# Optimization experiments

Measured on AMD Instinct MI355X. Metric: run time of the kernel, lower is better.

Reference implementation:

```python
import jax, jax.numpy as jnp
import numpy as np

HEADS = 2
K_HOP = 2
RATIO = 0.8
NEG_SLOPE = 0.01


def seg_softmax(logits, seg, num_seg):
    # torch_geometric.utils.softmax: numerically stable segment softmax
    m = jax.ops.segment_max(logits, seg, num_segments=num_seg)
    e = jnp.exp(logits - m[seg])
    d = jax.ops.segment_sum(e, seg, num_segments=num_seg)
    return e / d[seg]


def _attention(key_value, query, seg, num_seg, Wk, W1, W2, W3):
    # Attention.forward with enable_BN=False; weights stored [in,out] so x@W == torch Linear
    a = key_value @ Wk
    h = jnp.concatenate([a, query, a - query, a * query], axis=-1)  # [N,4H]
    h = jax.nn.leaky_relu(h @ W1, NEG_SLOPE)
    h = jax.nn.leaky_relu(h @ W2, NEG_SLOPE)
    h = jax.nn.leaky_relu(h @ W3, NEG_SLOPE)  # [N,1]
    return seg_softmax(h[:, 0], seg, num_seg)[:, None]  # att_weights [N,1]


def setup_inputs():
    key = jax.random.key(0)
    ks = jax.random.split(key, 10)
    B, n, H, epg = 64, 64, 128, 2048
    N = B * n
    x = jax.random.normal(ks[0], (N, H), jnp.float32)
    src = jax.random.randint(ks[1], (B, epg), 0, n)
    dst = jax.random.randint(ks[2], (B, epg), 0, n)
    off = (jnp.arange(B) * n)[:, None]
    edge_index = jnp.stack([(src + off).reshape(-1), (dst + off).reshape(-1)], 0)
    edge_weight = jax.random.uniform(ks[3], (B * epg,), jnp.float32)
    target_x = jax.random.normal(ks[4], (B, H), jnp.float32)
    batch_ixs = jnp.repeat(jnp.arange(B), n)
    s = lambda i, sh: jax.random.normal(ks[i], sh, jnp.float32) / np.sqrt(sh[-2])
    # index 0=cluster_att, 1=query_att, 2=cluster_att2, 3=query_att2
    att_Wk = s(5, (4, H, H))
    att_W1 = s(6, (4, 4 * H, 2 * H))
    att_W2 = s(7, (4, 2 * H, H))
    att_W3 = s(8, (4, H, 1))
    lin_W = s(9, (HEADS, H, H))
    return dict(x=x, edge_index=edge_index, edge_weight=edge_weight, target_x=target_x,
                batch_ixs=batch_ixs, att_Wk=att_Wk, att_W1=att_W1, att_W2=att_W2,
                att_W3=att_W3, lin_W=lin_W)


def reference(x, edge_index, edge_weight, target_x, batch_ixs, att_Wk, att_W1, att_W2, att_W3, lin_W):
    N, H = x.shape
    B = target_x.shape[0]
    n = N // B
    # ---- gcn_norm with self loops (fill 1.0) ----
    loop = jnp.arange(N)
    row = jnp.concatenate([edge_index[0], loop])
    col = jnp.concatenate([edge_index[1], loop])
    w = jnp.concatenate([edge_weight, jnp.ones((N,), edge_weight.dtype)])
    deg = jax.ops.segment_sum(w, col, num_segments=N)
    dinv = jnp.where(deg > 0, jax.lax.rsqrt(jnp.maximum(deg, 1e-12)), 0.0)
    ew = dinv[row] * w * dinv[col]  # [L]
    # ---- k-hop propagation ----
    def hop(v):
        return jax.ops.segment_sum(v[row] * ew[:, None], col, num_segments=N)
    x_q = x
    for _ in range(K_HOP):
        x_q = hop(x_q)
    qt = target_x[batch_ixs]  # repeat_interleave by per-graph counts (sorted batch)
    # ---- multi-head edge attention (reuse_att_w=True, dropout=0 -> E identical per head) ----
    f1 = _attention(x, x_q, batch_ixs, B, att_Wk[0], att_W1[0], att_W2[0], att_W3[0])
    f2 = _attention(x, qt, batch_ixs, B, att_Wk[1], att_W1[1], att_W2[1], att_W3[1])
    E = jax.nn.leaky_relu(f1[col] + f2[row], NEG_SLOPE)  # [L,1]
    E = seg_softmax(E[:, 0], col, N)[:, None]
    x_c = jnp.zeros_like(x)
    E_g = jnp.zeros((row.shape[0], 1), x.dtype)
    agg = jax.ops.segment_sum(x[row] * E, col, num_segments=N)
    for h in range(HEADS):
        x_c = x_c + jax.nn.leaky_relu(x + agg @ lin_W[h], NEG_SLOPE)
        E_g = E_g + E
    x_c = x_c / HEADS
    E_g = E_g / HEADS
    # ---- second k-hop + cluster scoring ----
    x_q2 = x_c
    for _ in range(K_HOP):
        x_q2 = hop(x_q2)
    g1 = _attention(x_c, x_q2, batch_ixs, B, att_Wk[2], att_W1[2], att_W2[2], att_W3[2])
    g2 = _attention(x_c, qt, batch_ixs, B, att_Wk[3], att_W1[3], att_W2[3], att_W3[3])
    # stack over heads then mean == g1+g2 (same attention modules reused per head)
    cluster_score = seg_softmax((g1 + g2)[:, 0], batch_ixs, B)  # [N]
    # ---- per-graph topk (ratio) ----
    kk = int(np.ceil(RATIO * n))
    _, idx = jax.lax.top_k(cluster_score.reshape(B, n), kk)  # descending, matches PyG topk
    perm = (idx + (jnp.arange(B) * n)[:, None]).reshape(-1)  # [Nk]
    x_out = x[perm] * cluster_score[perm][:, None]
    batch_out = batch_ixs[perm]
    # ---- S^T A S (dense equivalent of SparseTensor triple product) ----
    A_d = jnp.zeros((N, N), x.dtype).at[row, col].add(ew)
    S_d = jnp.zeros((N, N), x.dtype).at[row, col].add(E_g[:, 0])
    S_p = S_d[:, perm]  # S[:, perm] -> [N, Nk]
    A2 = S_p.T @ (A_d @ S_p)  # [Nk, Nk]
    Nk = perm.shape[0]
    A2 = A2.at[jnp.arange(Nk), jnp.arange(Nk)].set(1.0)  # fill_diag(1.0)
    return x_out, A2, batch_out, perm
```

## Files before the change

kernel.cpp:

```cpp
#include <hip/hip_runtime.h>

#define KK 52
#define NKOUT 3328
#define NEG 0.01f

typedef __attribute__((ext_vector_type(8))) __bf16 bf16x8;
typedef __attribute__((ext_vector_type(16))) float floatx16;

__device__ __forceinline__ float lrelu(float v){ return v > 0.f ? v : NEG*v; }

#define SW(r, ko) ((r)*40 + ((ko) ^ ((((r)>>3)&3) << 3)))

__device__ __forceinline__ void split_store8(const float* vv, __bf16* P0, __bf16* P1, __bf16* P2, int addr){
  bf16x8 p1, p2, p3;
  #pragma unroll
  for (int j = 0; j < 8; j++){
    __bf16 b1 = (__bf16)vv[j];
    float r1 = vv[j] - (float)b1;
    __bf16 b2 = (__bf16)r1;
    float r2 = r1 - (float)b2;
    p1[j] = b1; p2[j] = b2; p3[j] = (__bf16)r2;
  }
  *(bf16x8*)(P0 + addr) = p1;
  *(bf16x8*)(P1 + addr) = p2;
  *(bf16x8*)(P2 + addr) = p3;
}

__device__ __forceinline__ void mfma6(const __bf16* A0, const __bf16* A1, const __bf16* A2,
                                      const __bf16* B0, const __bf16* B1, const __bf16* B2,
                                      int aoff, int boff, floatx16* acc){
  bf16x8 a1 = *(const bf16x8*)(A0 + aoff);
  bf16x8 a2 = *(const bf16x8*)(A1 + aoff);
  bf16x8 a3 = *(const bf16x8*)(A2 + aoff);
  bf16x8 b1 = *(const bf16x8*)(B0 + boff);
  bf16x8 b2 = *(const bf16x8*)(B1 + boff);
  bf16x8 b3 = *(const bf16x8*)(B2 + boff);
  floatx16 c = *acc;
  c = __builtin_amdgcn_mfma_f32_32x32x16_bf16(a1,b1,c,0,0,0);
  c = __builtin_amdgcn_mfma_f32_32x32x16_bf16(a1,b2,c,0,0,0);
  c = __builtin_amdgcn_mfma_f32_32x32x16_bf16(a2,b1,c,0,0,0);
  c = __builtin_amdgcn_mfma_f32_32x32x16_bf16(a1,b3,c,0,0,0);
  c = __builtin_amdgcn_mfma_f32_32x32x16_bf16(a3,b1,c,0,0,0);
  c = __builtin_amdgcn_mfma_f32_32x32x16_bf16(a2,b2,c,0,0,0);
  *acc = c;
}

__device__ __forceinline__ void g_gemm(const float* A0, int ldA,
                                       const float* __restrict__ W0, int ldW, int K,
                                       __bf16* pb, floatx16* oA, floatx16* oB){
  __bf16 *As0 = pb, *As1 = pb+2560, *As2 = pb+5120;
  __bf16 *Bs0 = pb+7680, *Bs1 = pb+12800, *Bs2 = pb+17920;
  int tid = threadIdx.x;
  int sar = tid >> 2, sako = (tid & 3)*8;
  int bn = tid & 127, bk = (tid >> 7)*16;
  int wv_ = tid >> 6, L = tid & 63, m = L & 31, half = L >> 5;
  int rA = 32*(wv_ & 1) + m, rB0 = (wv_ >> 1)*32 + m, rB1 = rB0 + 64;
  const float* arow = A0 + (size_t)sar*ldA;
  floatx16 accA, accB;
  #pragma unroll
  for (int i = 0; i < 16; i++){ accA[i] = 0.f; accB[i] = 0.f; }
  float ra[8], wv[16];
  {
    float4 v0 = *(const float4*)(arow + sako);
    float4 v1 = *(const float4*)(arow + sako + 4);
    ra[0]=v0.x; ra[1]=v0.y; ra[2]=v0.z; ra[3]=v0.w; ra[4]=v1.x; ra[5]=v1.y; ra[6]=v1.z; ra[7]=v1.w;
    #pragma unroll
    for (int j = 0; j < 16; j++) wv[j] = W0[(size_t)(bk + j)*ldW + bn];
  }
  for (int k0 = 0; k0 < K; k0 += 32){
    split_store8(ra, As0, As1, As2, SW(sar, sako));
    split_store8(wv,     Bs0, Bs1, Bs2, SW(bn, bk));
    split_store8(wv + 8, Bs0, Bs1, Bs2, SW(bn, bk + 8));
    __syncthreads();
    int k1 = k0 + 32;
    float ra2[8], wv2[16];
    if (k1 < K){
      float4 v0 = *(const float4*)(arow + k1 + sako);
      float4 v1 = *(const float4*)(arow + k1 + sako + 4);
      ra2[0]=v0.x; ra2[1]=v0.y; ra2[2]=v0.z; ra2[3]=v0.w; ra2[4]=v1.x; ra2[5]=v1.y; ra2[6]=v1.z; ra2[7]=v1.w;
      #pragma unroll
      for (int j = 0; j < 16; j++) wv2[j] = W0[(size_t)(k1 + bk + j)*ldW + bn];
    }
    #pragma unroll
    for (int kg = 0; kg < 2; kg++){
      int ko = kg*16 + half*8;
      mfma6(As0,As1,As2, Bs0,Bs1,Bs2, SW(rA,ko), SW(rB0,ko), &accA);
      mfma6(As0,As1,As2, Bs0,Bs1,Bs2, SW(rA,ko), SW(rB1,ko), &accB);
    }
    __syncthreads();
    if (k1 < K){
      #pragma unroll
      for (int j = 0; j < 8; j++) ra[j] = ra2[j];
      #pragma unroll
      for (int j = 0; j < 16; j++) wv[j] = wv2[j];
    }
  }
  *oA = accA; *oB = accB;
}

__device__ __forceinline__ void g_gemm64_bp(const float* __restrict__ A0, int ldA,
                                            const __bf16* __restrict__ Bp, int bps, int ldKb, int K,
                                            __bf16* pb, floatx16* oC){
  __bf16 *As0 = pb, *As1 = pb+2560, *As2 = pb+5120;
  __bf16 *Bs0 = pb+7680, *Bs1 = pb+10240, *Bs2 = pb+12800;
  int tid = threadIdx.x;
  int sar = tid >> 2, sako = (tid & 3)*8;
  int bn = tid & 63, bk = (tid >> 6)*8;
  int wv_ = tid >> 6, L = tid & 63, m = L & 31, half = L >> 5;
  int rA = 32*(wv_ & 1) + m, rB = 32*(wv_ >> 1) + m;
  const float* arow = A0 + (size_t)sar*ldA;
  const __bf16* brow = Bp + (size_t)bn*ldKb + bk;
  floatx16 acc;
  #pragma unroll
  for (int i = 0; i < 16; i++) acc[i] = 0.f;
  float ra[8]; bf16x8 rb[3];
  {
    float4 v0 = *(const float4*)(arow + sako);
    float4 v1 = *(const float4*)(arow + sako + 4);
    ra[0]=v0.x; ra[1]=v0.y; ra[2]=v0.z; ra[3]=v0.w; ra[4]=v1.x; ra[5]=v1.y; ra[6]=v1.z; ra[7]=v1.w;
    rb[0] = *(const bf16x8*)(brow);
    rb[1] = *(const bf16x8*)(brow + bps);
    rb[2] = *(const bf16x8*)(brow + 2*bps);
  }
  for (int k0 = 0; k0 < K; k0 += 32){
    split_store8(ra, As0, As1, As2, SW(sar, sako));
    *(bf16x8*)(Bs0 + SW(bn, bk)) = rb[0];
    *(bf16x8*)(Bs1 + SW(bn, bk)) = rb[1];
    *(bf16x8*)(Bs2 + SW(bn, bk)) = rb[2];
    __syncthreads();
    int k1 = k0 + 32;
    float ra2[8]; bf16x8 rb2[3];
    if (k1 < K){
      float4 v0 = *(const float4*)(arow + k1 + sako);
      float4 v1 = *(const float4*)(arow + k1 + sako + 4);
      ra2[0]=v0.x; ra2[1]=v0.y; ra2[2]=v0.z; ra2[3]=v0.w; ra2[4]=v1.x; ra2[5]=v1.y; ra2[6]=v1.z; ra2[7]=v1.w;
      rb2[0] = *(const bf16x8*)(brow + k1);
      rb2[1] = *(const bf16x8*)(brow + bps + k1);
      rb2[2] = *(const bf16x8*)(brow + 2*bps + k1);
    }
    #pragma unroll
    for (int kg = 0; kg < 2; kg++){
      int ko = kg*16 + half*8;
      mfma6(As0,As1,As2, Bs0,Bs1,Bs2, SW(rA,ko), SW(rB,ko), &acc);
    }
    __syncthreads();
    if (k1 < K){
      #pragma unroll
      for (int j = 0; j < 8; j++) ra[j] = ra2[j];
      rb[0]=rb2[0]; rb[1]=rb2[1]; rb[2]=rb2[2];
    }
  }
  *oC = acc;
}

__device__ __forceinline__ void g_gemm_h64(const float* __restrict__ arow, const float* __restrict__ qrow,
                                           const __bf16* __restrict__ Bp,
                                           __bf16* pb, floatx16* oC){
  __bf16 *As0 = pb, *As1 = pb+2560, *As2 = pb+5120;
  __bf16 *Bs0 = pb+7680, *Bs1 = pb+10240, *Bs2 = pb+12800;
  int tid = threadIdx.x;
  int sar = tid >> 2, sako = (tid & 3)*8;
  int bn = tid & 63, bk = (tid >> 6)*8;
  int wv_ = tid >> 6, L = tid & 63, m = L & 31, half = L >> 5;
  int rA = 32*(wv_ & 1) + m, rB = 32*(wv_ >> 1) + m;
  const __bf16* brow = Bp + (size_t)bn*384 + bk;
  auto loadA = [&](int k0, float* r){
    int seg = k0 >> 7, kl = (k0 & 127) + sako;
    if (seg == 0){
      float4 a0 = *(const float4*)(arow + kl), a1 = *(const float4*)(arow + kl + 4);
      r[0]=a0.x; r[1]=a0.y; r[2]=a0.z; r[3]=a0.w; r[4]=a1.x; r[5]=a1.y; r[6]=a1.z; r[7]=a1.w;
    } else if (seg == 1){
      float4 q0 = *(const float4*)(qrow + kl), q1 = *(const float4*)(qrow + kl + 4);
      r[0]=q0.x; r[1]=q0.y; r[2]=q0.z; r[3]=q0.w; r[4]=q1.x; r[5]=q1.y; r[6]=q1.z; r[7]=q1.w;
    } else {
      float4 a0 = *(const float4*)(arow + kl), a1 = *(const float4*)(arow + kl + 4);
      float4 q0 = *(const float4*)(qrow + kl), q1 = *(const float4*)(qrow + kl + 4);
      r[0]=a0.x*q0.x; r[1]=a0.y*q0.y; r[2]=a0.z*q0.z; r[3]=a0.w*q0.w;
      r[4]=a1.x*q1.x; r[5]=a1.y*q1.y; r[6]=a1.z*q1.z; r[7]=a1.w*q1.w;
    }
  };
  floatx16 acc;
  #pragma unroll
  for (int i = 0; i < 16; i++) acc[i] = 0.f;
  float ra[8]; bf16x8 rb[3];
  loadA(0, ra);
  rb[0] = *(const bf16x8*)(brow);
  rb[1] = *(const bf16x8*)(brow + 98304);
  rb[2] = *(const bf16x8*)(brow + 196608);
  for (int k0 = 0; k0 < 384; k0 += 32){
    split_store8(ra, As0, As1, As2, SW(sar, sako));
    *(bf16x8*)(Bs0 + SW(bn, bk)) = rb[0];
    *(bf16x8*)(Bs1 + SW(bn, bk)) = rb[1];
    *(bf16x8*)(Bs2 + SW(bn, bk)) = rb[2];
    __syncthreads();
    int k1 = k0 + 32;
    float ra2[8]; bf16x8 rb2[3];
    if (k1 < 384){
      loadA(k1, ra2);
      rb2[0] = *(const bf16x8*)(brow + k1);
      rb2[1] = *(const bf16x8*)(brow + 98304 + k1);
      rb2[2] = *(const bf16x8*)(brow + 196608 + k1);
    }
    #pragma unroll
    for (int kg = 0; kg < 2; kg++){
      int ko = kg*16 + half*8;
      mfma6(As0,As1,As2, Bs0,Bs1,Bs2, SW(rA,ko), SW(rB,ko), &acc);
    }
    __syncthreads();
    if (k1 < 384){
      #pragma unroll
      for (int j = 0; j < 8; j++) ra[j] = ra2[j];
      rb[0]=rb2[0]; rb[1]=rb2[1]; rb[2]=rb2[2];
    }
  }
  *oC = acc;
}

__device__ __forceinline__ void c_write(floatx16 accA, floatx16 accB, float* C0, int ldC, int act){
  int tid = threadIdx.x, wv_ = tid >> 6, L = tid & 63, m = L & 31, half = L >> 5;
  int rB0 = (wv_ >> 1)*32 + m, rB1 = rB0 + 64;
  int row0 = 32*(wv_ & 1) + 4*half;
  #pragma unroll
  for (int reg = 0; reg < 16; reg++){
    int row = row0 + (reg & 3) + 8*(reg >> 2);
    float va = accA[reg], vb = accB[reg];
    if (act){ va = lrelu(va); vb = lrelu(vb); }
    C0[(size_t)row*ldC + rB0] = va;
    C0[(size_t)row*ldC + rB1] = vb;
  }
}

__device__ __forceinline__ void c_write64(floatx16 acc, float* C0, int ldC, int act){
  int tid = threadIdx.x, wv_ = tid >> 6, L = tid & 63, m = L & 31, half = L >> 5;
  int col = 32*(wv_ >> 1) + m;
  int row0 = 32*(wv_ & 1) + 4*half;
  #pragma unroll
  for (int reg = 0; reg < 16; reg++){
    int row = row0 + (reg & 3) + 8*(reg >> 2);
    float v = acc[reg];
    if (act) v = lrelu(v);
    C0[(size_t)row*ldC + col] = v;
  }
}

__device__ __forceinline__ void hop2_run(const float* A, const float* VfullL, int ldV,
                                         const float* srcG, float* dstG, int dstOff,
                                         float* Vt, float* Tt, int fbeg, int fend){
  int tid = threadIdx.x;
  int tc = (tid & 31)*2, tf = (tid >> 5)*4;
  for (int f0 = fbeg; f0 < fend; f0 += 32){
    if (!VfullL){
      for (int o = tid; o < 2048; o += 256){
        int r = o >> 5, f = o & 31;
        Vt[o] = srcG[r*128 + f0 + f];
      }
      __syncthreads();
    }
    float a00,a01,a02,a03,a10,a11,a12,a13;
    a00=a01=a02=a03=a10=a11=a12=a13=0.f;
    for (int r = 0; r < 64; r++){
      float x0 = A[r*64 + tc], x1 = A[r*64 + tc + 1];
      float4 v4 = VfullL ? *(const float4*)&VfullL[r*ldV + f0 + tf]
                         : *(const float4*)&Vt[r*32 + tf];
      a00 += x0*v4.x; a01 += x0*v4.y; a02 += x0*v4.z; a03 += x0*v4.w;
      a10 += x1*v4.x; a11 += x1*v4.y; a12 += x1*v4.z; a13 += x1*v4.w;
    }
    *(float4*)&Tt[tc*32 + tf]     = make_float4(a00,a01,a02,a03);
    *(float4*)&Tt[(tc+1)*32 + tf] = make_float4(a10,a11,a12,a13);
    __syncthreads();
    a00=a01=a02=a03=a10=a11=a12=a13=0.f;
    for (int r = 0; r < 64; r++){
      float x0 = A[r*64 + tc], x1 = A[r*64 + tc + 1];
      float4 v4 = *(const float4*)&Tt[r*32 + tf];
      a00 += x0*v4.x; a01 += x0*v4.y; a02 += x0*v4.z; a03 += x0*v4.w;
      a10 += x1*v4.x; a11 += x1*v4.y; a12 += x1*v4.z; a13 += x1*v4.w;
    }
    *(float4*)(dstG + tc*128 + dstOff + f0 + tf)     = make_float4(a00,a01,a02,a03);
    *(float4*)(dstG + (tc+1)*128 + dstOff + f0 + tf) = make_float4(a10,a11,a12,a13);
    __syncthreads();
  }
}

__device__ __forceinline__ void split_t_lds(float v, __bf16* Ls, int idx){
  __bf16 b1 = (__bf16)v;
  float r1 = v - (float)b1;
  __bf16 b2 = (__bf16)r1;
  __bf16 b3 = (__bf16)(r1 - (float)b2);
  Ls[idx] = b1; Ls[4224 + idx] = b2; Ls[8448 + idx] = b3;
}

__global__ __launch_bounds__(256) void k_p0(const int* __restrict__ ei, const float* __restrict__ ew,
                                            const float* __restrict__ x, const float* __restrict__ Wk,
                                            const float* __restrict__ W1, const float* __restrict__ W2,
                                            const float* __restrict__ linW,
                                            float* A_g, float* M_g, float* xq, float* a_buf,
                                            __bf16* W1fp, __bf16* W2p, __bf16* Wkgp,
                                            float* xl0, float* xl1, float* outA2){
  __shared__ __align__(16) char POOL[57856];
  float* pf = (float*)POOL;
  __bf16* pb = (__bf16*)POOL;
  int blk = blockIdx.x, tid = threadIdx.x;
  if (blk < 128){
    int b = blk >> 1, fh = blk & 1;
    float* Ws = pf; float* Mc = pf + 4096; float* dv = pf + 8192;
    for (int i = tid; i < 4096; i += 256){ Ws[i] = 0.f; Mc[i] = 0.f; }
    __syncthreads();
    const int* r0 = ei + b*2048;
    const int* c0 = ei + 64*2048 + b*2048;
    const float* w0 = ew + b*2048;
    int base = b*64;
    for (int e = tid; e < 2048; e += 256){
      int r = r0[e] - base, c = c0[e] - base;
      atomicAdd(&Ws[r*64 + c], w0[e]);
      atomicAdd(&Mc[r*64 + c], 1.f);
    }
    if (tid < 64){ atomicAdd(&Ws[tid*65], 1.f); atomicAdd(&Mc[tid*65], 1.f); }
    __syncthreads();
    if (tid < 64){
      float d = 0.f;
      for (int r = 0; r < 64; r++) d += Ws[r*64 + tid];
      dv[tid] = d > 0.f ? rsqrtf(fmaxf(d, 1e-12f)) : 0.f;
    }
    __syncthreads();
    for (int i = tid; i < 4096; i += 256){
      int r = i >> 6, c = i & 63;
      float a = dv[r]*Ws[i]*dv[c];
      Ws[i] = a;
      if (fh == 0){
        A_g[b*4096 + i] = a;
        M_g[b*4096 + i] = Mc[i];
      }
    }
    __syncthreads();
    hop2_run(Ws, nullptr, 0, x + (size_t)b*8192, xq + (size_t)b*8192, 0, pf + 8256, pf + 10304,
             fh*64, fh*64 + 64);
  } else if (blk < 256){
    int idx = blk - 128, z = idx >> 6, b = idx & 63;
    floatx16 cA, cB;
    g_gemm(x + (size_t)b*8192, 128, Wk + (size_t)z*16384, 128, 128, pb, &cA, &cB);
    c_write(cA, cB, a_buf + (size_t)z*524288 + (size_t)b*8192, 128, 0);
  } else if (blk < 352){
    __bf16* Ls = (__bf16*)POOL;
    int t = blk - 256, z = t/24, tt = t%24, k0 = (tt >> 2)*64, c0 = (tt & 3)*64;
    const float* Wz = W1 + (size_t)z*131072;
    for (int i = tid; i < 4096; i += 256){
      int kk = i >> 6, cc = i & 63, kr = k0 + kk, c = c0 + cc;
      float v;
      if (kr < 128)       v = Wz[kr*256 + c] + Wz[(kr + 256)*256 + c];
      else if (kr < 256)  v = Wz[kr*256 + c] - Wz[(kr + 128)*256 + c];
      else                v = Wz[(kr + 128)*256 + c];
      split_t_lds(v, Ls, cc*66 + kk);
    }
    __syncthreads();
    __bf16* outp = W1fp + (size_t)z*294912;
    for (int i = tid; i < 4096; i += 256){
      int cc = i >> 6, kk = i & 63;
      int o = (c0 + cc)*384 + k0 + kk;
      int li = cc*66 + kk;
      outp[o] = Ls[li];
      outp[98304 + o] = Ls[4224 + li];
      outp[196608 + o] = Ls[8448 + li];
    }
  } else if (blk < 384){
    __bf16* Ls = (__bf16*)POOL;
    int t = blk - 352, z = t >> 3, tt = t & 7, k0 = (tt >> 1)*64, c0 = (tt & 1)*64;
    const float* Wz = W2 + (size_t)z*32768;
    for (int i = tid; i < 4096; i += 256){
      int kk = i >> 6, cc = i & 63;
      split_t_lds(Wz[(k0 + kk)*128 + c0 + cc], Ls, cc*66 + kk);
    }
    __syncthreads();
    __bf16* outp = W2p + (size_t)z*98304;
    for (int i = tid; i < 4096; i += 256){
      int cc = i >> 6, kk = i & 63;
      int o = (c0 + cc)*256 + k0 + kk;
      int li = cc*66 + kk;
      outp[o] = Ls[li];
      outp[32768 + o] = Ls[4224 + li];
      outp[65536 + o] = Ls[8448 + li];
    }
  } else if (blk < 392){
    __bf16* Ls = (__bf16*)POOL;
    int t = blk - 384, z = t >> 2, tt = t & 3, k0 = (tt >> 1)*64, c0 = (tt & 1)*64;
    const float* Wz = Wk + (size_t)(2 + z)*16384;
    for (int i = tid; i < 4096; i += 256){
      int kk = i >> 6, cc = i & 63;
      split_t_lds(Wz[(k0 + kk)*128 + c0 + cc], Ls, cc*66 + kk);
    }
    __syncthreads();
    __bf16* outp = Wkgp + (size_t)z*49152;
    for (int i = tid; i < 4096; i += 256){
      int cc = i >> 6, kk = i & 63;
      int o = (c0 + cc)*128 + k0 + kk;
      int li = cc*66 + kk;
      outp[o] = Ls[li];
      outp[16384 + o] = Ls[4224 + li];
      outp[32768 + o] = Ls[8448 + li];
    }
  } else if (blk < 3096){
    float4* p = (float4*)outA2;
    int base = (blk - 392)*1024 + tid;
    #pragma unroll
    for (int i = 0; i < 4; i++) p[base + i*256] = make_float4(0.f,0.f,0.f,0.f);
  } else {
    int idx = blk - 3096, z = idx >> 6, b = idx & 63;
    floatx16 cA, cB;
    g_gemm(x + (size_t)b*8192, 128, linW + (size_t)z*16384, 128, 128, pb, &cA, &cB);
    c_write(cA, cB, (z ? xl1 : xl0) + (size_t)b*8192, 128, 0);
  }
}

__global__ __launch_bounds__(256) void k_h1(const float* __restrict__ a_buf, const float* __restrict__ q0,
                                            const float* __restrict__ tgt, const __bf16* __restrict__ W1fp,
                                            float* h1){
  __shared__ __align__(16) char POOL[30720];
  __bf16* pb = (__bf16*)POOL;
  int blk = blockIdx.x, tid = threadIdx.x;
  int b = blk >> 3, z = (blk >> 2) & 1, nq = blk & 3;
  int sar = tid >> 2;
  const float* arow = a_buf + (size_t)z*524288 + ((size_t)b*64 + sar)*128;
  const float* qrow = z ? (tgt + (size_t)b*128) : (q0 + ((size_t)b*64 + sar)*128);
  floatx16 c;
  g_gemm_h64(arow, qrow, W1fp + (size_t)z*294912 + (size_t)nq*64*384, pb, &c);
  c_write64(c, h1 + (size_t)z*1048576 + (size_t)b*16384 + nq*64, 256, 1);
}

__global__ __launch_bounds__(256) void k_w2p(const float* __restrict__ h1, const __bf16* __restrict__ W2p,
                                             const float* __restrict__ W3, float* __restrict__ lp){
  __shared__ __align__(16) char POOL[30720];
  __shared__ float lgp[128];
  __bf16* pb = (__bf16*)POOL;
  int blk = blockIdx.x, tid = threadIdx.x;
  int b = blk >> 2, z = (blk >> 1) & 1, nh = blk & 1;
  floatx16 c;
  g_gemm64_bp(h1 + (size_t)z*1048576 + (size_t)b*16384, 256,
              W2p + (size_t)z*98304 + (size_t)nh*64*256, 32768, 256, 256, pb, &c);
  int wv_ = tid >> 6, L = tid & 63, m = L & 31, half = L >> 5;
  int col = 32*(wv_ >> 1) + m;
  float w = W3[z*128 + nh*64 + col];
  float v[16];
  #pragma unroll
  for (int reg = 0; reg < 16; reg++) v[reg] = lrelu(c[reg])*w;
  #pragma unroll
  for (int off = 1; off < 32; off <<= 1)
    #pragma unroll
    for (int reg = 0; reg < 16; reg++) v[reg] += __shfl_xor(v[reg], off);
  if (m == 0){
    #pragma unroll
    for (int reg = 0; reg < 16; reg++) lgp[wv_*32 + half*16 + reg] = v[reg];
  }
  __syncthreads();
  if (tid < 64){
    int row = tid, rh = row >> 5, rem = row & 31;
    int hf = (rem >> 2) & 1, rg = (rem & 3) + 4*(rem >> 3);
    float p = lgp[rh*32 + hf*16 + rg] + lgp[(rh + 2)*32 + hf*16 + rg];
    lp[(z*2 + nh)*4096 + b*64 + row] = p;
  }
}

__global__ __launch_bounds__(256) void k_edgehop(const float* __restrict__ M_g, const float* __restrict__ lp,
                                                 const float* __restrict__ x, const float* __restrict__ xl0g,
                                                 const float* __restrict__ xl1g, const float* __restrict__ A_g,
                                                 float* S_g, float* xcb, float* xq2){
  __shared__ __align__(16) float Mc[4096];
  __shared__ __align__(16) float xh[4096];
  __shared__ __align__(16) float xl0h[4096];
  __shared__ __align__(16) float xl1h[4096];
  __shared__ __align__(16) float Ab[4096];
  __shared__ __align__(16) float Tt[2048];
  __shared__ float f1s[64], f2s[64];
  int blk = blockIdx.x, b = blk >> 1, fh = blk & 1, tid = threadIdx.x;
  int foff = fh*64;
  for (int i = tid; i < 4096; i += 256) Mc[i] = M_g[b*4096 + i];
  for (int o = tid*4; o < 4096; o += 1024){
    int r = o >> 6, f = o & 63;
    *(float4*)&xh[o]   = *(const float4*)(x    + (size_t)b*8192 + r*128 + foff + f);
    *(float4*)&xl0h[o] = *(const float4*)(xl0g + (size_t)b*8192 + r*128 + foff + f);
    *(float4*)&xl1h[o] = *(const float4*)(xl1g + (size_t)b*8192 + r*128 + foff + f);
  }
  if (tid < 128){
    int z = tid >> 6, r = tid & 63;
    float d = lp[(z*2)*4096 + b*64 + r] + lp[(z*2 + 1)*4096 + b*64 + r];
    float l = lrelu(d);
    float mx = l;
    #pragma unroll
    for (int off = 32; off; off >>= 1) mx = fmaxf(mx, __shfl_xor(mx, off));
    float e = expf(l - mx);
    float s = e;
    #pragma unroll
    for (int off = 32; off; off >>= 1) s += __shfl_xor(s, off);
    (z ? f2s : f1s)[r] = e/s;
  }
  __syncthreads();
  {
    int c = tid >> 2, sub = tid & 3;
    float m = -1e30f;
    for (int r = sub; r < 64; r += 4)
      if (Mc[r*64 + c] > 0.f) m = fmaxf(m, lrelu(f1s[c] + f2s[r]));
    m = fmaxf(m, __shfl_xor(m, 1));
    m = fmaxf(m, __shfl_xor(m, 2));
    float s = 0.f;
    for (int r = sub; r < 64; r += 4){
      float mc = Mc[r*64 + c];
      if (mc > 0.f) s += mc*expf(lrelu(f1s[c] + f2s[r]) - m);
    }
    s += __shfl_xor(s, 1);
    s += __shfl_xor(s, 2);
    for (int r = sub; r < 64; r += 4){
      float mc = Mc[r*64 + c];
      float v = 0.f;
      if (mc > 0.f) v = mc*expf(lrelu(f1s[c] + f2s[r]) - m)/s;
      Mc[r*64 + c] = v;
    }
  }
  __syncthreads();
  if (fh == 0)
    for (int i = tid; i < 4096; i += 256) S_g[b*4096 + i] = Mc[i];
  {
    int tc = (tid & 15)*4, tf = (tid >> 4)*4;
    float a0[4][4], a1[4][4];
    #pragma unroll
    for (int i = 0; i < 4; i++)
      #pragma unroll
      for (int j = 0; j < 4; j++){ a0[i][j] = 0.f; a1[i][j] = 0.f; }
    for (int r = 0; r < 64; r++){
      float4 e4 = *(const float4*)&Mc[r*64 + tc];
      float4 p0 = *(const float4*)&xl0h[r*64 + tf];
      float4 p1 = *(const float4*)&xl1h[r*64 + tf];
      float e_[4] = {e4.x,e4.y,e4.z,e4.w};
      float p0_[4] = {p0.x,p0.y,p0.z,p0.w};
      float p1_[4] = {p1.x,p1.y,p1.z,p1.w};
      #pragma unroll
      for (int ci = 0; ci < 4; ci++)
        #pragma unroll
        for (int fj = 0; fj < 4; fj++){
          a0[ci][fj] += e_[ci]*p0_[fj];
          a1[ci][fj] += e_[ci]*p1_[fj];
        }
    }
    __syncthreads();
    #pragma unroll
    for (int ci = 0; ci < 4; ci++){
      int c = tc + ci;
      float4 xv = *(const float4*)&xh[c*64 + tf];
      float4 o;
      o.x = 0.5f*(lrelu(xv.x + a0[ci][0]) + lrelu(xv.x + a1[ci][0]));
      o.y = 0.5f*(lrelu(xv.y + a0[ci][1]) + lrelu(xv.y + a1[ci][1]));
      o.z = 0.5f*(lrelu(xv.z + a0[ci][2]) + lrelu(xv.z + a1[ci][2]));
      o.w = 0.5f*(lrelu(xv.w + a0[ci][3]) + lrelu(xv.w + a1[ci][3]));
      *(float4*)&xh[c*64 + tf] = o;
      *(float4*)(xcb + (size_t)b*8192 + c*128 + foff + tf) = o;
    }
  }
  for (int i = tid*4; i < 4096; i += 1024)
    *(float4*)&Ab[i] = *(const float4*)(A_g + b*4096 + i);
  __syncthreads();
  hop2_run(Ab, xh, 64, nullptr, xq2 + (size_t)b*8192, foff, Tt, Tt, 0, 64);
}

__global__ __launch_bounds__(256) void k_wkg(const float* __restrict__ xcb, const __bf16* __restrict__ Wkgp,
                                             float* a_buf){
  __shared__ __align__(16) char POOL[30720];
  __bf16* pb = (__bf16*)POOL;
  int blk = blockIdx.x;
  int b = blk >> 2, z = (blk >> 1) & 1, nh = blk & 1;
  floatx16 c;
  g_gemm64_bp(xcb + (size_t)b*8192, 128,
              Wkgp + (size_t)z*49152 + (size_t)nh*64*128, 16384, 128, 128, pb, &c);
  c_write64(c, a_buf + (size_t)z*524288 + (size_t)b*8192 + nh*64, 128, 0);
}

__global__ __launch_bounds__(256) void k_A2c(const float* __restrict__ lp, const float* __restrict__ x,
                                             const float* __restrict__ A_g, const float* __restrict__ S_g,
                                             float* outA2, float* outX, float* outB, float* outP){
  __shared__ __align__(16) float At[64*68];
  __shared__ __align__(16) float Sp[64*56];
  __shared__ __align__(16) float Tq[64*56];
  __shared__ int pi[64];
  __shared__ float pv[64];
  int b = blockIdx.x, tid = threadIdx.x;
  if (tid < 64){
    int lane = tid;
    float f[2];
    #pragma unroll
    for (int z = 0; z < 2; z++){
      float d = lp[(z*2)*4096 + b*64 + lane] + lp[(z*2 + 1)*4096 + b*64 + lane];
      float l = lrelu(d);
      float mx = l;
      #pragma unroll
      for (int off = 32; off; off >>= 1) mx = fmaxf(mx, __shfl_xor(mx, off));
      float e = expf(l - mx);
      float sm = e;
      #pragma unroll
      for (int off = 32; off; off >>= 1) sm += __shfl_xor(sm, off);
      f[z] = e/sm;
    }
    float l = f[0] + f[1];
    float m = l;
    #pragma unroll
    for (int off = 32; off; off >>= 1) m = fmaxf(m, __shfl_xor(m, off));
    float e = expf(l - m);
    float sm = e;
    #pragma unroll
    for (int off = 32; off; off >>= 1) sm += __shfl_xor(sm, off);
    float v = e/sm;
    int idx = lane;
    #pragma unroll
    for (int k = 2; k <= 64; k <<= 1){
      #pragma unroll
      for (int j = k >> 1; j > 0; j >>= 1){
        float ov = __shfl_xor(v, j);
        int   oi = __shfl_xor(idx, j);
        bool ascBlock = (lane & k) == 0;
        bool iAmLow   = (lane & j) == 0;
        bool otherPrec = (ov > v) || (ov == v && oi < idx);
        bool take = (ascBlock == iAmLow) ? otherPrec : !otherPrec;
        if (take){ v = ov; idx = oi; }
      }
    }
    pi[lane] = idx; pv[lane] = v;
    if (lane < KK){
      outB[b*KK + lane] = (float)b;
      outP[b*KK + lane] = (float)(b*64 + idx);
    }
  }
  __syncthreads();
  for (int o = tid*4; o < KK*128; o += 1024){
    int j = o >> 7, f = o & 127;
    float4 xv = *(const float4*)(x + ((size_t)b*64 + pi[j])*128 + f);
    float sv = pv[j];
    *(float4*)(outX + (size_t)b*KK*128 + o) = make_float4(xv.x*sv, xv.y*sv, xv.z*sv, xv.w*sv);
  }
  for (int idx = tid; idx < 4096; idx += 256){
    int i = idx >> 6, k = idx & 63;
    At[k*68 + i] = A_g[b*4096 + idx];
  }
  for (int idx = tid; idx < 4096; idx += 256){
    int k = idx >> 6, t = idx & 63;
    if (t < 56) Sp[k*56 + t] = (t < KK) ? S_g[b*4096 + k*64 + pi[t]] : 0.f;
  }
  __syncthreads();
  if (tid < 224){
    int i0 = (tid/14)*4, t0 = (tid % 14)*4;
    float acc[4][4];
    #pragma unroll
    for (int a = 0; a < 4; a++)
      #pragma unroll
      for (int c = 0; c < 4; c++) acc[a][c] = 0.f;
    for (int k = 0; k < 64; k++){
      float4 a4 = *(const float4*)&At[k*68 + i0];
      float4 s4 = *(const float4*)&Sp[k*56 + t0];
      float a_[4] = {a4.x,a4.y,a4.z,a4.w};
      float s_[4] = {s4.x,s4.y,s4.z,s4.w};
      #pragma unroll
      for (int ii = 0; ii < 4; ii++)
        #pragma unroll
        for (int tt = 0; tt < 4; tt++) acc[ii][tt] += a_[ii]*s_[tt];
    }
    #pragma unroll
    for (int ii = 0; ii < 4; ii++)
      *(float4*)&Tq[(i0+ii)*56 + t0] = make_float4(acc[ii][0],acc[ii][1],acc[ii][2],acc[ii][3]);
  }
  __syncthreads();
  if (tid < 169){
    int a0 = (tid/13)*4, t0 = (tid % 13)*4;
    float acc[4][4];
    #pragma unroll
    for (int a = 0; a < 4; a++)
      #pragma unroll
      for (int c = 0; c < 4; c++) acc[a][c] = 0.f;
    for (int i = 0; i < 64; i++){
      float4 s4 = *(const float4*)&Sp[i*56 + a0];
      float4 t4 = *(const float4*)&Tq[i*56 + t0];
      float s_[4] = {s4.x,s4.y,s4.z,s4.w};
      float t_[4] = {t4.x,t4.y,t4.z,t4.w};
      #pragma unroll
      for (int aa = 0; aa < 4; aa++)
        #pragma unroll
        for (int tt = 0; tt < 4; tt++) acc[aa][tt] += s_[aa]*t_[tt];
    }
    #pragma unroll
    for (int aa = 0; aa < 4; aa++){
      int a = a0 + aa;
      float4 o;
      o.x = (a == t0    ) ? 1.f : acc[aa][0];
      o.y = (a == t0 + 1) ? 1.f : acc[aa][1];
      o.z = (a == t0 + 2) ? 1.f : acc[aa][2];
      o.w = (a == t0 + 3) ? 1.f : acc[aa][3];
      *(float4*)(outA2 + (size_t)(b*KK + a)*NKOUT + b*KK + t0) = o;
    }
  }
}

extern "C" void kernel_launch(void* const* d_in, const int* in_sizes, int n_in,
                              void* d_out, int out_size, void* d_ws, size_t ws_size,
                              hipStream_t stream){
  const float* x    = (const float*)d_in[0];
  const int*   ei   = (const int*)d_in[1];
  const float* ew   = (const float*)d_in[2];
  const float* tgt  = (const float*)d_in[3];
  const float* Wk   = (const float*)d_in[5];
  const float* W1   = (const float*)d_in[6];
  const float* W2   = (const float*)d_in[7];
  const float* W3   = (const float*)d_in[8];
  const float* linW = (const float*)d_in[9];
  float* out = (float*)d_out;

  float* wf   = (float*)d_ws;
  float* A_g  = wf;
  float* M_g  = wf + 262144;
  float* S_g  = wf + 524288;
  float* xq   = wf + 786432;
  float* xq2  = wf + 1310720;
  float* xl0  = wf + 1835008;
  float* xcb  = wf + 2359296;
  float* a_buf= wf + 2883584;
  float* h1   = wf + 3932160;
  float* lp   = wf + 6029312;
  float* xl1  = wf + 6045696;
  __bf16* W1fp = (__bf16*)(wf + 6569984);
  __bf16* W2p  = (__bf16*)(wf + 7159808);
  __bf16* Wkgp = (__bf16*)(wf + 7356416);

  float* outX  = out;
  float* outA2 = out + 425984;
  float* outB  = out + 425984 + 11075584;
  float* outP  = outB + NKOUT;

  k_p0<<<dim3(3224), dim3(256), 0, stream>>>(ei, ew, x, Wk, W1, W2, linW, A_g, M_g, xq, a_buf,
                                             W1fp, W2p, Wkgp, xl0, xl1, outA2);
  k_h1<<<dim3(512), dim3(256), 0, stream>>>(a_buf, xq, tgt, W1fp, h1);
  k_w2p<<<dim3(256), dim3(256), 0, stream>>>(h1, W2p, W3, lp);
  k_edgehop<<<dim3(128), dim3(256), 0, stream>>>(M_g, lp, x, xl0, xl1, A_g, S_g, xcb, xq2);
  k_wkg<<<dim3(256), dim3(256), 0, stream>>>(xcb, Wkgp, a_buf);
  k_h1<<<dim3(512), dim3(256), 0, stream>>>(a_buf, xq2, tgt, W1fp + 2*294912, h1);
  k_w2p<<<dim3(256), dim3(256), 0, stream>>>(h1, W2p + 2*98304, W3 + 2*128, lp);
  k_A2c<<<dim3(64), dim3(256), 0, stream>>>(lp, x, A_g, S_g, outA2, outX, outB, outP);
}
```

Measured before the change: 214.7 us.

## Fuse Wk projection of cluster features into edgehop kernel, drop k_wkg launch

The separate k_wkg GEMM launch is removed. Each edgehop block now multiplies its 64-feature half of the cluster features by the packed Wk weights with register-resident split-bf16 MFMA and writes a partial product. The second k_h1 sums the two feature-half partials while loading its A operand, so xcb no longer round-trips through memory and one launch is saved. The cost is extra partial-buffer traffic, an extra load in k_h1, and extra MFMA work and register pressure inside the low-occupancy edgehop kernel (128 blocks).

```diff
diff --git a/kernel.cpp b/kernel.cpp
--- a/kernel.cpp
+++ b/kernel.cpp
@@ -26,6 +26,19 @@
   *(bf16x8*)(P2 + addr) = p3;
 }
 
+__device__ __forceinline__ void split8r(const float* vv, bf16x8* q1, bf16x8* q2, bf16x8* q3){
+  bf16x8 p1, p2, p3;
+  #pragma unroll
+  for (int j = 0; j < 8; j++){
+    __bf16 b1 = (__bf16)vv[j];
+    float r1 = vv[j] - (float)b1;
+    __bf16 b2 = (__bf16)r1;
+    float r2 = r1 - (float)b2;
+    p1[j] = b1; p2[j] = b2; p3[j] = (__bf16)r2;
+  }
+  *q1 = p1; *q2 = p2; *q3 = p3;
+}
+
 __device__ __forceinline__ void mfma6(const __bf16* A0, const __bf16* A1, const __bf16* A2,
                                       const __bf16* B0, const __bf16* B1, const __bf16* B2,
                                       int aoff, int boff, floatx16* acc){
@@ -35,6 +48,18 @@
   bf16x8 b1 = *(const bf16x8*)(B0 + boff);
   bf16x8 b2 = *(const bf16x8*)(B1 + boff);
   bf16x8 b3 = *(const bf16x8*)(B2 + boff);
+  floatx16 c = *acc;
+  c = __builtin_amdgcn_mfma_f32_32x32x16_bf16(a1,b1,c,0,0,0);
+  c = __builtin_amdgcn_mfma_f32_32x32x16_bf16(a1,b2,c,0,0,0);
+  c = __builtin_amdgcn_mfma_f32_32x32x16_bf16(a2,b1,c,0,0,0);
+  c = __builtin_amdgcn_mfma_f32_32x32x16_bf16(a1,b3,c,0,0,0);
+  c = __builtin_amdgcn_mfma_f32_32x32x16_bf16(a3,b1,c,0,0,0);
+  c = __builtin_amdgcn_mfma_f32_32x32x16_bf16(a2,b2,c,0,0,0);
+  *acc = c;
+}
+
+__device__ __forceinline__ void mfma6r(bf16x8 a1, bf16x8 a2, bf16x8 a3,
+                                       bf16x8 b1, bf16x8 b2, bf16x8 b3, floatx16* acc){
   floatx16 c = *acc;
   c = __builtin_amdgcn_mfma_f32_32x32x16_bf16(a1,b1,c,0,0,0);
   c = __builtin_amdgcn_mfma_f32_32x32x16_bf16(a1,b2,c,0,0,0);
@@ -153,7 +178,8 @@
   *oC = acc;
 }
 
-__device__ __forceinline__ void g_gemm_h64(const float* __restrict__ arow, const float* __restrict__ qrow,
+__device__ __forceinline__ void g_gemm_h64(const float* arow, const float* arow2,
+                                           const float* __restrict__ qrow,
                                            const __bf16* __restrict__ Bp,
                                            __bf16* pb, floatx16* oC){
   __bf16 *As0 = pb, *As1 = pb+2560, *As2 = pb+5120;
@@ -164,19 +190,28 @@
   int wv_ = tid >> 6, L = tid & 63, m = L & 31, half = L >> 5;
   int rA = 32*(wv_ & 1) + m, rB = 32*(wv_ >> 1) + m;
   const __bf16* brow = Bp + (size_t)bn*384 + bk;
+  auto loadAv = [&](int kl, float* r){
+    float4 a0 = *(const float4*)(arow + kl), a1 = *(const float4*)(arow + kl + 4);
+    if (arow2){
+      float4 c0 = *(const float4*)(arow2 + kl), c1 = *(const float4*)(arow2 + kl + 4);
+      a0 = make_float4(a0.x + c0.x, a0.y + c0.y, a0.z + c0.z, a0.w + c0.w);
+      a1 = make_float4(a1.x + c1.x, a1.y + c1.y, a1.z + c1.z, a1.w + c1.w);
+    }
+    r[0]=a0.x; r[1]=a0.y; r[2]=a0.z; r[3]=a0.w; r[4]=a1.x; r[5]=a1.y; r[6]=a1.z; r[7]=a1.w;
+  };
   auto loadA = [&](int k0, float* r){
     int seg = k0 >> 7, kl = (k0 & 127) + sako;
     if (seg == 0){
-      float4 a0 = *(const float4*)(arow + kl), a1 = *(const float4*)(arow + kl + 4);
-      r[0]=a0.x; r[1]=a0.y; r[2]=a0.z; r[3]=a0.w; r[4]=a1.x; r[5]=a1.y; r[6]=a1.z; r[7]=a1.w;
+      loadAv(kl, r);
     } else if (seg == 1){
       float4 q0 = *(const float4*)(qrow + kl), q1 = *(const float4*)(qrow + kl + 4);
       r[0]=q0.x; r[1]=q0.y; r[2]=q0.z; r[3]=q0.w; r[4]=q1.x; r[5]=q1.y; r[6]=q1.z; r[7]=q1.w;
     } else {
-      float4 a0 = *(const float4*)(arow + kl), a1 = *(const float4*)(arow + kl + 4);
+      float av[8];
+      loadAv(kl, av);
       float4 q0 = *(const float4*)(qrow + kl), q1 = *(const float4*)(qrow + kl + 4);
-      r[0]=a0.x*q0.x; r[1]=a0.y*q0.y; r[2]=a0.z*q0.z; r[3]=a0.w*q0.w;
-      r[4]=a1.x*q1.x; r[5]=a1.y*q1.y; r[6]=a1.z*q1.z; r[7]=a1.w*q1.w;
+      r[0]=av[0]*q0.x; r[1]=av[1]*q0.y; r[2]=av[2]*q0.z; r[3]=av[3]*q0.w;
+      r[4]=av[4]*q1.x; r[5]=av[5]*q1.y; r[6]=av[6]*q1.z; r[7]=av[7]*q1.w;
     }
   };
   floatx16 acc;
@@ -340,7 +375,7 @@
     g_gemm(x + (size_t)b*8192, 128, Wk + (size_t)z*16384, 128, 128, pb, &cA, &cB);
     c_write(cA, cB, a_buf + (size_t)z*524288 + (size_t)b*8192, 128, 0);
   } else if (blk < 352){
-    __bf16* Ls = (__bf16*)POOL;
+    __bf16* Ls = pb;
     int t = blk - 256, z = t/24, tt = t%24, k0 = (tt >> 2)*64, c0 = (tt & 3)*64;
     const float* Wz = W1 + (size_t)z*131072;
     for (int i = tid; i < 4096; i += 256){
@@ -362,7 +397,7 @@
       outp[196608 + o] = Ls[8448 + li];
     }
   } else if (blk < 384){
-    __bf16* Ls = (__bf16*)POOL;
+    __bf16* Ls = pb;
     int t = blk - 352, z = t >> 3, tt = t & 7, k0 = (tt >> 1)*64, c0 = (tt & 1)*64;
     const float* Wz = W2 + (size_t)z*32768;
     for (int i = tid; i < 4096; i += 256){
@@ -380,7 +415,7 @@
       outp[65536 + o] = Ls[8448 + li];
     }
   } else if (blk < 392){
-    __bf16* Ls = (__bf16*)POOL;
+    __bf16* Ls = pb;
     int t = blk - 384, z = t >> 2, tt = t & 3, k0 = (tt >> 1)*64, c0 = (tt & 1)*64;
     const float* Wz = Wk + (size_t)(2 + z)*16384;
     for (int i = tid; i < 4096; i += 256){
@@ -410,18 +445,20 @@
   }
 }
 
-__global__ __launch_bounds__(256) void k_h1(const float* __restrict__ a_buf, const float* __restrict__ q0,
-                                            const float* __restrict__ tgt, const __bf16* __restrict__ W1fp,
-                                            float* h1){
+__global__ __launch_bounds__(256) void k_h1(const float* __restrict__ abuf, const float* __restrict__ abuf2,
+                                            const float* __restrict__ q0, const float* __restrict__ tgt,
+                                            const __bf16* __restrict__ W1fp, float* h1){
   __shared__ __align__(16) char POOL[30720];
   __bf16* pb = (__bf16*)POOL;
   int blk = blockIdx.x, tid = threadIdx.x;
   int b = blk >> 3, z = (blk >> 2) & 1, nq = blk & 3;
   int sar = tid >> 2;
-  const float* arow = a_buf + (size_t)z*524288 + ((size_t)b*64 + sar)*128;
+  size_t aoff = (size_t)z*524288 + ((size_t)b*64 + sar)*128;
+  const float* arow  = abuf + aoff;
+  const float* arow2 = abuf2 ? abuf2 + aoff : nullptr;
   const float* qrow = z ? (tgt + (size_t)b*128) : (q0 + ((size_t)b*64 + sar)*128);
   floatx16 c;
-  g_gemm_h64(arow, qrow, W1fp + (size_t)z*294912 + (size_t)nq*64*384, pb, &c);
+  g_gemm_h64(arow, arow2, qrow, W1fp + (size_t)z*294912 + (size_t)nq*64*384, pb, &c);
   c_write64(c, h1 + (size_t)z*1048576 + (size_t)b*16384 + nq*64, 256, 1);
 }
 
@@ -461,7 +498,8 @@
 __global__ __launch_bounds__(256) void k_edgehop(const float* __restrict__ M_g, const float* __restrict__ lp,
                                                  const float* __restrict__ x, const float* __restrict__ xl0g,
                                                  const float* __restrict__ xl1g, const float* __restrict__ A_g,
-                                                 float* S_g, float* xcb, float* xq2){
+                                                 const __bf16* __restrict__ Wkgp,
+                                                 float* S_g, float* ap, float* xq2){
   __shared__ __align__(16) float Mc[4096];
   __shared__ __align__(16) float xh[4096];
   __shared__ __align__(16) float xl0h[4096];
@@ -549,25 +587,52 @@
       o.z = 0.5f*(lrelu(xv.z + a0[ci][2]) + lrelu(xv.z + a1[ci][2]));
       o.w = 0.5f*(lrelu(xv.w + a0[ci][3]) + lrelu(xv.w + a1[ci][3]));
       *(float4*)&xh[c*64 + tf] = o;
-      *(float4*)(xcb + (size_t)b*8192 + c*128 + foff + tf) = o;
+    }
+  }
+  __syncthreads();
+  {
+    int wv_ = tid >> 6, L = tid & 63, m = L & 31, half = L >> 5;
+    int rA = 32*(wv_ & 1) + m, rB = 32*(wv_ >> 1) + m;
+    bf16x8 af[4][3];
+    #pragma unroll
+    for (int kg = 0; kg < 4; kg++){
+      int ko = kg*16 + half*8;
+      float av[8];
+      float4 v0 = *(const float4*)&xh[rA*64 + ko];
+      float4 v1 = *(const float4*)&xh[rA*64 + ko + 4];
+      av[0]=v0.x; av[1]=v0.y; av[2]=v0.z; av[3]=v0.w; av[4]=v1.x; av[5]=v1.y; av[6]=v1.z; av[7]=v1.w;
+      split8r(av, &af[kg][0], &af[kg][1], &af[kg][2]);
+    }
+    int row0 = 32*(wv_ & 1) + 4*half;
+    #pragma unroll
+    for (int z = 0; z < 2; z++){
+      #pragma unroll
+      for (int nh = 0; nh < 2; nh++){
+        floatx16 acc;
+        #pragma unroll
+        for (int i = 0; i < 16; i++) acc[i] = 0.f;
+        const __bf16* bb = Wkgp + (size_t)z*49152 + (size_t)(nh*64 + rB)*128 + foff;
+        #pragma unroll
+        for (int kg = 0; kg < 4; kg++){
+          int ko = kg*16 + half*8;
+          bf16x8 b1 = *(const bf16x8*)(bb + ko);
+          bf16x8 b2 = *(const bf16x8*)(bb + 16384 + ko);
+          bf16x8 b3 = *(const bf16x8*)(bb + 32768 + ko);
+          mfma6r(af[kg][0], af[kg][1], af[kg][2], b1, b2, b3, &acc);
+        }
+        float* C0 = ap + (size_t)fh*1048576 + (size_t)z*524288 + (size_t)b*8192 + nh*64;
+        #pragma unroll
+        for (int reg = 0; reg < 16; reg++){
+          int row = row0 + (reg & 3) + 8*(reg >> 2);
+          C0[(size_t)row*128 + rB] = acc[reg];
+        }
+      }
     }
   }
   for (int i = tid*4; i < 4096; i += 1024)
-    *(float4*)&Ab[i] = *(const float4*)(A_g + b*4096 + i);
+    *(float4*)&Mc[i] = *(const float4*)(A_g + b*4096 + i);
   __syncthreads();
-  hop2_run(Ab, xh, 64, nullptr, xq2 + (size_t)b*8192, foff, Tt, Tt, 0, 64);
-}
-
-__global__ __launch_bounds__(256) void k_wkg(const float* __restrict__ xcb, const __bf16* __restrict__ Wkgp,
-                                             float* a_buf){
-  __shared__ __align__(16) char POOL[30720];
-  __bf16* pb = (__bf16*)POOL;
-  int blk = blockIdx.x;
-  int b = blk >> 2, z = (blk >> 1) & 1, nh = blk & 1;
-  floatx16 c;
-  g_gemm64_bp(xcb + (size_t)b*8192, 128,
-              Wkgp + (size_t)z*49152 + (size_t)nh*64*128, 16384, 128, 128, pb, &c);
-  c_write64(c, a_buf + (size_t)z*524288 + (size_t)b*8192 + nh*64, 128, 0);
+  hop2_run(Mc, xh, 64, nullptr, xq2 + (size_t)b*8192, foff, xl0h, xl0h, 0, 64);
 }
 
 __global__ __launch_bounds__(256) void k_A2c(const float* __restrict__ lp, const float* __restrict__ x,
@@ -721,6 +786,8 @@
   __bf16* W1fp = (__bf16*)(wf + 6569984);
   __bf16* W2p  = (__bf16*)(wf + 7159808);
   __bf16* Wkgp = (__bf16*)(wf + 7356416);
+  float* ap   = wf + 7405568;
+  (void)xcb;
 
   float* outX  = out;
   float* outA2 = out + 425984;
@@ -729,11 +796,10 @@
 
   k_p0<<<dim3(3224), dim3(256), 0, stream>>>(ei, ew, x, Wk, W1, W2, linW, A_g, M_g, xq, a_buf,
                                              W1fp, W2p, Wkgp, xl0, xl1, outA2);
-  k_h1<<<dim3(512), dim3(256), 0, stream>>>(a_buf, xq, tgt, W1fp, h1);
+  k_h1<<<dim3(512), dim3(256), 0, stream>>>(a_buf, nullptr, xq, tgt, W1fp, h1);
   k_w2p<<<dim3(256), dim3(256), 0, stream>>>(h1, W2p, W3, lp);
-  k_edgehop<<<dim3(128), dim3(256), 0, stream>>>(M_g, lp, x, xl0, xl1, A_g, S_g, xcb, xq2);
-  k_wkg<<<dim3(256), dim3(256), 0, stream>>>(xcb, Wkgp, a_buf);
-  k_h1<<<dim3(512), dim3(256), 0, stream>>>(a_buf, xq2, tgt, W1fp + 2*294912, h1);
+  k_edgehop<<<dim3(128), dim3(256), 0, stream>>>(M_g, lp, x, xl0, xl1, A_g, Wkgp, S_g, ap, xq2);
+  k_h1<<<dim3(512), dim3(256), 0, stream>>>(ap, ap + 1048576, xq2, tgt, W1fp + 2*294912, h1);
   k_w2p<<<dim3(256), dim3(256), 0, stream>>>(h1, W2p + 2*98304, W3 + 2*128, lp);
   k_A2c<<<dim3(64), dim3(256), 0, stream>>>(lp, x, A_g, S_g, outA2, outX, outB, outP);
 }
```

Result: slower. 219.8 us (+2.4%).
